# Performance work log

Measured on AMD Instinct MI355X. Metric: run time of the kernel, lower is better.

The kernel has to match this reference:

```python
import jax, jax.numpy as jnp
import numpy as np

N_NODES = 100000


def setup_inputs() -> dict:
    key = jax.random.key(0)
    k1, k2, k3, k4, k5 = jax.random.split(key, 5)
    n_edges = 3200000
    in_f, out_f = 256, 256
    X = jax.random.normal(k1, (N_NODES, in_f), dtype=jnp.float32)
    edge_src = jax.random.randint(k2, (n_edges,), 0, N_NODES, dtype=jnp.int32)
    edge_dst = jax.random.randint(k3, (n_edges,), 0, N_NODES, dtype=jnp.int32)
    edge_val = jax.random.uniform(k4, (n_edges,), dtype=jnp.float32)
    # kaiming-uniform-like init for weight (out_f, in_f)
    bound = np.sqrt(6.0 / in_f)
    W = jax.random.uniform(k5, (out_f, in_f), dtype=jnp.float32, minval=-bound, maxval=bound)
    b = jnp.zeros((out_f,), dtype=jnp.float32)
    return {"X": X, "edge_src": edge_src, "edge_dst": edge_dst,
            "edge_val": edge_val, "W": W, "b": b}


def reference(X, edge_src, edge_dst, edge_val, W, b):
    # S = A @ X, where A is COO sparse: A[src, dst] = val
    # gather neighbor features, scale by edge value, scatter-add to src rows
    msgs = edge_val[:, None] * X[edge_dst]              # [E, in_f]
    S = jax.ops.segment_sum(msgs, edge_src, num_segments=N_NODES)  # [N, in_f]
    # dense projection + bias: (A X) W^T + b
    return S @ W.T + b
```

## Files before the change

kernel.cpp:

```cpp
#include <hip/hip_runtime.h>

#define NNODES 100000
#define F 256
#define NBKT ((NNODES + 127) / 128)
#define BKT_CAP 5120
#define CHUNK_A 8192

typedef unsigned short u16;
typedef unsigned int   u32;
typedef __attribute__((ext_vector_type(8))) short short8v;
typedef __attribute__((ext_vector_type(8))) unsigned short ushort8;
typedef __attribute__((ext_vector_type(4))) float f32x4;

__device__ __forceinline__ u16 f2bf(float f) {
    u32 u = __float_as_uint(f);
    u32 r = u + 0x7FFFu + ((u >> 16) & 1u);
    return (u16)(r >> 16);
}
__device__ __forceinline__ float bf2f(u16 h) {
    return __uint_as_float(((u32)h) << 16);
}

__global__ __launch_bounds__(256) void cast_w(const float* __restrict__ W,
                                              u16* __restrict__ Wb) {
    int i = blockIdx.x * 256 + threadIdx.x;
    if (i >= F * F / 4) return;
    float4 w = ((const float4*)W)[i];
    ushort4 o;
    o.x = f2bf(w.x); o.y = f2bf(w.y); o.z = f2bf(w.z); o.w = f2bf(w.w);
    ((ushort4*)Wb)[i] = o;
}

__global__ __launch_bounds__(256) void cast_x(const float* __restrict__ X,
                                              u16* __restrict__ Xb, int total4) {
    int i = blockIdx.x * 256 + threadIdx.x;
    if (i >= total4) return;
    float4 x = ((const float4*)X)[i];
    ushort4 o;
    o.x = f2bf(x.x); o.y = f2bf(x.y); o.z = f2bf(x.z); o.w = f2bf(x.w);
    ((ushort4*)Xb)[i] = o;
}

__global__ __launch_bounds__(256) void gemm_mfma(const u16* __restrict__ Xb,
                                                 const u16* __restrict__ Wb,
                                                 u16* __restrict__ Yb) {
    const int wave = threadIdx.x >> 6;
    const int lane = threadIdx.x & 63;
    const int lm   = lane & 15;
    const int kg   = lane >> 4;
    const int m0   = blockIdx.x * 128 + wave * 32;
    const int n0   = blockIdx.y * 128;

    f32x4 acc[2][8];
#pragma unroll
    for (int t = 0; t < 2; ++t)
#pragma unroll
        for (int u = 0; u < 8; ++u) acc[t][u] = (f32x4){0.f, 0.f, 0.f, 0.f};

    int rowA[2];
#pragma unroll
    for (int t = 0; t < 2; ++t) {
        int row = m0 + t * 16 + lm;
        rowA[t] = (row < NNODES) ? row : NNODES - 1;
    }

    for (int k0 = 0; k0 < F; k0 += 32) {
        const int kb = k0 + kg * 8;
        short8v aF[2];
#pragma unroll
        for (int t = 0; t < 2; ++t)
            aF[t] = *(const short8v*)(Xb + (size_t)rowA[t] * F + kb);
        short8v bF[8];
#pragma unroll
        for (int u = 0; u < 8; ++u)
            bF[u] = *(const short8v*)(Wb + (size_t)(n0 + u * 16 + lm) * F + kb);
#pragma unroll
        for (int t = 0; t < 2; ++t)
#pragma unroll
            for (int u = 0; u < 8; ++u)
                acc[t][u] = __builtin_amdgcn_mfma_f32_16x16x32_bf16(aF[t], bF[u], acc[t][u], 0, 0, 0);
    }

#pragma unroll
    for (int t = 0; t < 2; ++t) {
        int rbase = m0 + t * 16 + kg * 4;
#pragma unroll
        for (int i = 0; i < 4; ++i) {
            int row = rbase + i;
            if (row < NNODES) {
#pragma unroll
                for (int u = 0; u < 8; ++u)
                    Yb[(size_t)row * F + n0 + u * 16 + lm] = f2bf(acc[t][u][i]);
            }
        }
    }
}

__global__ __launch_bounds__(256) void init_cur(int* __restrict__ cur) {
    int i = blockIdx.x * 256 + threadIdx.x;
    if (i < NBKT) cur[i] = i * BKT_CAP;
}

__global__ __launch_bounds__(256) void bin_edges(const int* __restrict__ src,
                                                 const int* __restrict__ dst,
                                                 const float* __restrict__ val,
                                                 int* __restrict__ cur,
                                                 int2* __restrict__ temp,
                                                 int n_edges) {
    __shared__ int hist[NBKT];
    __shared__ int bas[NBKT];
    const int e0 = blockIdx.x * CHUNK_A;
    for (int i = threadIdx.x; i < NBKT; i += 256) hist[i] = 0;
    __syncthreads();

    int lp[32];
#pragma unroll
    for (int k = 0; k < 32; ++k) {
        int e = e0 + k * 256 + threadIdx.x;
        if (e < n_edges) lp[k] = atomicAdd(&hist[src[e] >> 7], 1);
    }
    __syncthreads();
    for (int i = threadIdx.x; i < NBKT; i += 256) {
        int c = hist[i];
        bas[i] = c ? atomicAdd(&cur[i], c) : 0;
    }
    __syncthreads();
#pragma unroll
    for (int k = 0; k < 32; ++k) {
        int e = e0 + k * 256 + threadIdx.x;
        if (e < n_edges) {
            int s = src[e];
            int pos = bas[s >> 7] + lp[k];
            temp[pos] = make_int2(((s & 127) << 20) | dst[e], __float_as_int(val[e]));
        }
    }
}

__global__ __launch_bounds__(256) void sort_bucket(const int* __restrict__ cur,
                                                   const int2* __restrict__ temp,
                                                   int2* __restrict__ pack,
                                                   int2* __restrict__ nodeseg) {
    __shared__ int h[128];
    __shared__ int curl[128];
    const int b = blockIdx.x;
    const int base = b * BKT_CAP;
    const int cnt = cur[b] - base;
    const int tid = threadIdx.x;

    if (tid < 128) h[tid] = 0;
    __syncthreads();
    for (int j = tid; j < cnt; j += 256)
        atomicAdd(&h[temp[base + j].x >> 20], 1);
    __syncthreads();
    for (int off = 1; off < 128; off <<= 1) {
        int x = 0;
        if (tid < 128 && tid >= off) x = h[tid - off];
        __syncthreads();
        if (tid < 128) h[tid] += x;
        __syncthreads();
    }
    if (tid < 128) {
        int incl = h[tid];
        int prev = tid ? h[tid - 1] : 0;
        curl[tid] = base + prev;
        int node = b * 128 + tid;
        if (node < NNODES) nodeseg[node] = make_int2(base + prev, base + incl);
    }
    __syncthreads();
    for (int j = tid; j < cnt; j += 256) {
        int2 p = temp[base + j];
        int loc = p.x >> 20;
        int pos = atomicAdd(&curl[loc], 1);
        pack[pos] = make_int2(p.x & 0xFFFFF, p.y);
    }
}

__global__ __launch_bounds__(256) void gather_nodes(const int2* __restrict__ nodeseg,
                                                    const int2* __restrict__ pack,
                                                    const u16* __restrict__ Yb,
                                                    const float* __restrict__ bias,
                                                    float* __restrict__ out) {
    int node = blockIdx.x * 4 + (threadIdx.x >> 6);
    if (node >= NNODES) return;
    const int lane = threadIdx.x & 63;
    const int half = lane >> 5;
    const int l5   = lane & 31;

    int2 seg = nodeseg[node];
    const int beg = seg.x, end = seg.y;

    float acc[8];
#pragma unroll
    for (int i = 0; i < 8; ++i) acc[i] = 0.f;

    for (int j = beg; j < end; j += 16) {
        int dsts[8];
        float v[8];
        ushort8 y[8];
#pragma unroll
        for (int q = 0; q < 8; ++q) {
            int idx = j + 2 * q + half;
            int safe = idx < end ? idx : end - 1;
            long long raw = __builtin_nontemporal_load((const long long*)&pack[safe]);
            dsts[q] = (int)(raw & 0xFFFFFFFFll);
            v[q] = (idx < end) ? __int_as_float((int)(raw >> 32)) : 0.f;
        }
#pragma unroll
        for (int q = 0; q < 8; ++q)
            y[q] = *(const ushort8*)(Yb + (size_t)dsts[q] * F + l5 * 8);
#pragma unroll
        for (int q = 0; q < 8; ++q)
#pragma unroll
            for (int i = 0; i < 8; ++i)
                acc[i] += v[q] * bf2f(y[q][i]);
    }

#pragma unroll
    for (int i = 0; i < 8; ++i) acc[i] += __shfl_xor(acc[i], 32);

    const int col = l5 * 8 + half * 4;
    float4 bv = *(const float4*)&bias[col];
    f32x4 o;
    o[0] = acc[half * 4 + 0] + bv.x;
    o[1] = acc[half * 4 + 1] + bv.y;
    o[2] = acc[half * 4 + 2] + bv.z;
    o[3] = acc[half * 4 + 3] + bv.w;
    __builtin_nontemporal_store(o, (f32x4*)&out[(size_t)node * F + col]);
}

extern "C" void kernel_launch(void* const* d_in, const int* in_sizes, int n_in,
                              void* d_out, int out_size, void* d_ws, size_t ws_size,
                              hipStream_t stream) {
    const float* X        = (const float*)d_in[0];
    const int*   edge_src = (const int*)d_in[1];
    const int*   edge_dst = (const int*)d_in[2];
    const float* edge_val = (const float*)d_in[3];
    const float* W        = (const float*)d_in[4];
    const float* b        = (const float*)d_in[5];
    float*       out      = (float*)d_out;
    const int n_edges     = in_sizes[1];

    char* base = (char*)d_ws;
    const size_t ybBytes   = (size_t)NNODES * F * sizeof(u16);
    const size_t packBytes = (size_t)NBKT * BKT_CAP * sizeof(int2);
    u16*  Yb      = (u16*)base;
    int2* pack    = (int2*)(base + ybBytes);
    int2* temp    = (int2*)(base + ybBytes + packBytes);
    u16*  Xb      = (u16*)pack;
    u16*  Wb      = (u16*)(base + ybBytes + 2 * packBytes);
    int2* nodeseg = (int2*)((char*)Wb + (size_t)F * F * sizeof(u16));
    int*  cur     = (int*)(nodeseg + NNODES);

    cast_w<<<(F * F / 4 + 255) / 256, 256, 0, stream>>>(W, Wb);
    int xt4 = NNODES * F / 4;
    cast_x<<<(xt4 + 255) / 256, 256, 0, stream>>>(X, Xb, xt4);

    dim3 ggrid((NNODES + 127) / 128, F / 128);
    gemm_mfma<<<ggrid, 256, 0, stream>>>(Xb, Wb, Yb);

    init_cur<<<(NBKT + 255) / 256, 256, 0, stream>>>(cur);
    bin_edges<<<(n_edges + CHUNK_A - 1) / CHUNK_A, 256, 0, stream>>>(edge_src, edge_dst, edge_val,
                                                                     cur, temp, n_edges);
    sort_bucket<<<NBKT, 256, 0, stream>>>(cur, temp, pack, nodeseg);

    gather_nodes<<<(NNODES + 3) / 4, 256, 0, stream>>>(nodeseg, pack, Yb, b, out);
}
```

Before: 595.1 us.

## Prefetch edge packs, stage bucket in LDS, pack byte offsets, use packed FMA

The gather kernel now loads the next 16 edge records while the current rows are being accumulated, and stores destinations as precomputed byte offsets so the address math is shorter. It also accumulates with two-wide packed FMAs on bf16 pairs. The bucket sort keeps each bucket in shared memory so the temp array is read only once, and binning reads src only once by packing the bucket and local index into registers. The cost is more registers and a large LDS array in sort_bucket, which may lower occupancy. Edges beyond bucket capacity are now clamped.

New measurement: 599.8 us. No clear change (+0.8%).

```diff
diff --git a/kernel.cpp b/kernel.cpp
--- a/kernel.cpp
+++ b/kernel.cpp
@@ -11,14 +11,12 @@
 typedef __attribute__((ext_vector_type(8))) short short8v;
 typedef __attribute__((ext_vector_type(8))) unsigned short ushort8;
 typedef __attribute__((ext_vector_type(4))) float f32x4;
+typedef __attribute__((ext_vector_type(2))) float f32x2;
 
 __device__ __forceinline__ u16 f2bf(float f) {
     u32 u = __float_as_uint(f);
     u32 r = u + 0x7FFFu + ((u >> 16) & 1u);
     return (u16)(r >> 16);
-}
-__device__ __forceinline__ float bf2f(u16 h) {
-    return __uint_as_float(((u32)h) << 16);
 }
 
 __global__ __launch_bounds__(256) void cast_w(const float* __restrict__ W,
@@ -113,25 +111,32 @@
     for (int i = threadIdx.x; i < NBKT; i += 256) hist[i] = 0;
     __syncthreads();
 
-    int lp[32];
-#pragma unroll
-    for (int k = 0; k < 32; ++k) {
-        int e = e0 + k * 256 + threadIdx.x;
-        if (e < n_edges) lp[k] = atomicAdd(&hist[src[e] >> 7], 1);
-    }
-    __syncthreads();
-    for (int i = threadIdx.x; i < NBKT; i += 256) {
-        int c = hist[i];
-        bas[i] = c ? atomicAdd(&cur[i], c) : 0;
-    }
-    __syncthreads();
+    u32 lpk[32];
 #pragma unroll
     for (int k = 0; k < 32; ++k) {
         int e = e0 + k * 256 + threadIdx.x;
         if (e < n_edges) {
             int s = src[e];
-            int pos = bas[s >> 7] + lp[k];
-            temp[pos] = make_int2(((s & 127) << 20) | dst[e], __float_as_int(val[e]));
+            int bkt = s >> 7;
+            int l = atomicAdd(&hist[bkt], 1);
+            lpk[k] = (u32)l | ((u32)(s & 127) << 13) | ((u32)bkt << 20);
+        }
+    }
+    __syncthreads();
+    for (int i = threadIdx.x; i < NBKT; i += 256) {
+        int c = hist[i];
+        bas[i] = c ? atomicAdd(&cur[i], c) : 0;
+    }
+    __syncthreads();
+#pragma unroll
+    for (int k = 0; k < 32; ++k) {
+        int e = e0 + k * 256 + threadIdx.x;
+        if (e < n_edges) {
+            u32 p   = lpk[k];
+            int bkt = (int)(p >> 20);
+            int pos = bas[bkt] + (int)(p & 0x1FFFu);
+            int sl  = (int)((p >> 13) & 127u);
+            temp[pos] = make_int2((sl << 20) | dst[e], __float_as_int(val[e]));
         }
     }
 }
@@ -140,17 +145,22 @@
                                                    const int2* __restrict__ temp,
                                                    int2* __restrict__ pack,
                                                    int2* __restrict__ nodeseg) {
+    __shared__ int2 tl[BKT_CAP];
     __shared__ int h[128];
     __shared__ int curl[128];
     const int b = blockIdx.x;
     const int base = b * BKT_CAP;
-    const int cnt = cur[b] - base;
+    int cnt = cur[b] - base;
+    if (cnt > BKT_CAP) cnt = BKT_CAP;
     const int tid = threadIdx.x;
 
     if (tid < 128) h[tid] = 0;
     __syncthreads();
-    for (int j = tid; j < cnt; j += 256)
-        atomicAdd(&h[temp[base + j].x >> 20], 1);
+    for (int j = tid; j < cnt; j += 256) {
+        int2 t = temp[base + j];
+        tl[j] = t;
+        atomicAdd(&h[t.x >> 20], 1);
+    }
     __syncthreads();
     for (int off = 1; off < 128; off <<= 1) {
         int x = 0;
@@ -168,10 +178,10 @@
     }
     __syncthreads();
     for (int j = tid; j < cnt; j += 256) {
-        int2 p = temp[base + j];
+        int2 p = tl[j];
         int loc = p.x >> 20;
         int pos = atomicAdd(&curl[loc], 1);
-        pack[pos] = make_int2(p.x & 0xFFFFF, p.y);
+        pack[pos] = make_int2((p.x & 0xFFFFF) << 9, p.y);
     }
 }
 
@@ -185,36 +195,63 @@
     const int lane = threadIdx.x & 63;
     const int half = lane >> 5;
     const int l5   = lane & 31;
+    const u32 loff = (u32)l5 * 16u;
+    const char* Ybc = (const char*)Yb;
 
     int2 seg = nodeseg[node];
     const int beg = seg.x, end = seg.y;
 
-    float acc[8];
-#pragma unroll
-    for (int i = 0; i < 8; ++i) acc[i] = 0.f;
+    f32x2 acc2[4];
+#pragma unroll
+    for (int i = 0; i < 4; ++i) acc2[i] = (f32x2){0.f, 0.f};
+
+    long long pr[8];
+#pragma unroll
+    for (int q = 0; q < 8; ++q) {
+        int idx  = beg + 2 * q + half;
+        int safe = idx < end ? idx : beg;
+        pr[q] = __builtin_nontemporal_load((const long long*)&pack[safe]);
+    }
 
     for (int j = beg; j < end; j += 16) {
-        int dsts[8];
+        u32 off[8];
         float v[8];
-        ushort8 y[8];
 #pragma unroll
         for (int q = 0; q < 8; ++q) {
             int idx = j + 2 * q + half;
+            off[q] = (u32)((unsigned long long)pr[q] & 0xFFFFFFFFull);
+            v[q]   = (idx < end) ? __int_as_float((int)(pr[q] >> 32)) : 0.f;
+        }
+        ushort8 y[8];
+#pragma unroll
+        for (int q = 0; q < 8; ++q)
+            y[q] = *(const ushort8*)(Ybc + (off[q] + loff));
+        int jn = j + 16;
+#pragma unroll
+        for (int q = 0; q < 8; ++q) {
+            int idx  = jn + 2 * q + half;
             int safe = idx < end ? idx : end - 1;
-            long long raw = __builtin_nontemporal_load((const long long*)&pack[safe]);
-            dsts[q] = (int)(raw & 0xFFFFFFFFll);
-            v[q] = (idx < end) ? __int_as_float((int)(raw >> 32)) : 0.f;
-        }
-#pragma unroll
-        for (int q = 0; q < 8; ++q)
-            y[q] = *(const ushort8*)(Yb + (size_t)dsts[q] * F + l5 * 8);
-#pragma unroll
-        for (int q = 0; q < 8; ++q)
-#pragma unroll
-            for (int i = 0; i < 8; ++i)
-                acc[i] += v[q] * bf2f(y[q][i]);
-    }
-
+            pr[q] = __builtin_nontemporal_load((const long long*)&pack[safe]);
+        }
+        __builtin_amdgcn_sched_barrier(0);
+#pragma unroll
+        for (int q = 0; q < 8; ++q) {
+            f32x2 vv; vv[0] = v[q]; vv[1] = v[q];
+            const u32* yp = (const u32*)&y[q];
+#pragma unroll
+            for (int i = 0; i < 4; ++i) {
+                u32 pb = yp[i];
+                f32x2 yy;
+                yy[0] = __uint_as_float(pb << 16);
+                yy[1] = __uint_as_float(pb & 0xFFFF0000u);
+                acc2[i] = __builtin_elementwise_fma(yy, vv, acc2[i]);
+            }
+        }
+    }
+
+    float acc[8];
+#pragma unroll
+    for (int i = 0; i < 4; ++i) { acc[2 * i] = acc2[i][0]; acc[2 * i + 1] = acc2[i][1]; }
 #pragma unroll
     for (int i = 0; i < 8; ++i) acc[i] += __shfl_xor(acc[i], 32);
 
```
